# Optimization experiments

Measured on AMD Instinct MI355X. Metric: run time of the kernel, lower is better.

The kernel has to match this reference:

```python
import jax, jax.numpy as jnp
import numpy as np

N, E, D, H = 50000, 800000, 128, 8
DH = D // H  # 16
EPS_LN = 1e-5


def layer_norm(x, gamma, beta):
    mu = jnp.mean(x, axis=-1, keepdims=True)
    var = jnp.var(x, axis=-1, keepdims=True)
    return (x - mu) * jax.lax.rsqrt(var + EPS_LN) * gamma + beta


def setup_inputs() -> dict:
    key = jax.random.key(0)
    ks = jax.random.split(key, 12)
    s = 1.0 / np.sqrt(D)
    x = jax.random.normal(ks[0], (N, D), dtype=jnp.float32)
    src = jax.random.randint(ks[1], (E,), 0, N, dtype=jnp.int32)
    dst = jax.random.randint(ks[2], (E,), 0, N, dtype=jnp.int32)
    Wq = jax.random.normal(ks[3], (D, D), dtype=jnp.float32) * s
    Wk = jax.random.normal(ks[4], (D, D), dtype=jnp.float32) * s
    Wv = jax.random.normal(ks[5], (D, D), dtype=jnp.float32) * s
    Wo = jax.random.normal(ks[6], (D, D), dtype=jnp.float32) * s
    bq = jnp.zeros((D,), jnp.float32)
    bk = jnp.zeros((D,), jnp.float32)
    bv = jnp.zeros((D,), jnp.float32)
    bo = jnp.zeros((D,), jnp.float32)
    gamma1 = jnp.ones((D,), jnp.float32)
    beta1 = jnp.zeros((D,), jnp.float32)
    gamma2 = jnp.ones((D,), jnp.float32)
    beta2 = jnp.zeros((D,), jnp.float32)
    return dict(x=x, src=src, dst=dst, Wq=Wq, bq=bq, Wk=Wk, bk=bk, Wv=Wv, bv=bv,
                Wo=Wo, bo=bo, gamma1=gamma1, beta1=beta1, gamma2=gamma2, beta2=beta2)


def reference(x, src, dst, Wq, bq, Wk, bk, Wv, bv, Wo, bo, gamma1, beta1, gamma2, beta2):
    n = x.shape[0]
    Q = (x @ Wq + bq).reshape(n, H, DH)   # [N,H,Dh]
    K = (x @ Wk + bk).reshape(n, H, DH)
    V = (x @ Wv + bv).reshape(n, H, DH)
    # edge-wise QK dot: score[e,h] = sum_d K[src[e],h,d] * Q[dst[e],h,d]
    score = jnp.sum(K[src] * Q[dst], axis=-1) / np.sqrt(DH)  # [E,H]
    score = jnp.exp(jnp.clip(score, -5.0, 5.0))
    # scatter-sum weighted values and normalizer over destination nodes
    wV = jax.ops.segment_sum(V[src] * score[..., None], dst, num_segments=n)  # [N,H,Dh]
    z = jax.ops.segment_sum(score, dst, num_segments=n)                        # [N,H]
    attn = (wV / (z[..., None] + 1e-3)).reshape(n, D)
    h = layer_norm(x + attn, gamma1, beta1)
    # sublayer: h + relu(O(LN(h)))  (dropout = 0)
    h = h + jax.nn.relu(layer_norm(h, gamma2, beta2) @ Wo + bo)
    return h
```

## Files before the change

kernel.cpp:

```cpp
#include <hip/hip_runtime.h>

typedef unsigned short ushort_t;
typedef __attribute__((ext_vector_type(8))) short short8;
typedef __attribute__((ext_vector_type(4))) float floatx4;
typedef __attribute__((ext_vector_type(2))) _Float16 half2v;
typedef __attribute__((ext_vector_type(8))) _Float16 half8;

#define QSCALE 0.36067376022224085f
#define SCLIP  7.2134752044448170f

__device__ __forceinline__ unsigned h2u(half2v h) {
    union { half2v h; unsigned u; } x; x.h = h; return x.u;
}
__device__ __forceinline__ half2v u2h(unsigned u) {
    union { unsigned u; half2v h; } x; x.u = u; return x.h;
}
__device__ __forceinline__ ushort_t h2us(_Float16 h) {
    union { _Float16 h; ushort_t u; } x; x.h = h; return x.u;
}
__device__ __forceinline__ unsigned pkrtz(float a, float b) {
    auto h = __builtin_amdgcn_cvt_pkrtz(a, b);
    union { decltype(h) h2; unsigned u; } x; x.h2 = h; return x.u;
}
__device__ __forceinline__ float dot2h(half2v a, half2v b, float c) {
#if __has_builtin(__builtin_amdgcn_fdot2)
    return __builtin_amdgcn_fdot2(a, b, c, false);
#else
    return c + (float)a[0] * (float)b[0] + (float)a[1] * (float)b[1];
#endif
}
__device__ __forceinline__ half2v pk_shfl_add(half2v a, int m) {
    unsigned o = (unsigned)__shfl_xor((int)h2u(a), m, 64);
    return a + u2h(o);
}

__global__ __launch_bounds__(256) void transpose_swz(
    const float* __restrict__ Wq, const float* __restrict__ Wk,
    const float* __restrict__ Wv, const float* __restrict__ Wo,
    ushort_t* __restrict__ out, int* __restrict__ deg, int* __restrict__ gcount, int N)
{
    int flat = (blockIdx.y * gridDim.x + blockIdx.x) * 256 + threadIdx.x;
    if (flat == 0) *gcount = 0;
    for (int i = flat; i < N; i += 8192) deg[i] = 0;

    const float* W = (blockIdx.y == 0) ? Wq : (blockIdx.y == 1) ? Wk :
                     (blockIdx.y == 2) ? Wv : Wo;
    ushort_t* T = out + (size_t)blockIdx.y * 128 * 128;
    int t = blockIdx.x * 256 + threadIdx.x;
    int kg = t >> 7;
    int n  = t & 127;
    int k0 = kg * 8;
    float w[8];
    #pragma unroll
    for (int j = 0; j < 8; j++)
        w[j] = W[(size_t)(k0 + j) * 128 + n];
    int4 o;
    o.x = (int)pkrtz(w[0], w[1]);
    o.y = (int)pkrtz(w[2], w[3]);
    o.z = (int)pkrtz(w[4], w[5]);
    o.w = (int)pkrtz(w[6], w[7]);
    int sn = n >> 4, l15 = n & 15, kb = kg >> 2, quad = kg & 3;
    size_t f = ((size_t)((sn * 4 + kb) * 4 + quad)) * 128 + (size_t)l15 * 8;
    *(int4*)(T + f) = o;
}

__global__ __launch_bounds__(512, 8) void gemm_qkv(
    const float* __restrict__ X, const ushort_t* __restrict__ Wsw,
    const float* __restrict__ bq, const float* __restrict__ bk, const float* __restrict__ bv,
    ushort_t* __restrict__ Q, ushort_t* __restrict__ KV, int M,
    const int* __restrict__ dst, int* __restrict__ deg, int* __restrict__ rank, int E)
{
    __shared__ ushort_t Xs[32 * 136];
    __shared__ ushort_t Cs[32 * 392];
    int tid = threadIdx.x;
    int rowBase = blockIdx.x * 32;

    {
        int nblk = gridDim.x;
        int fb = blockIdx.x;
        int per = (E + nblk - 1) / nblk;
        int end = min(per * (fb + 1), E);
        for (int i = per * fb + tid; i < end; i += 512)
            rank[i] = atomicAdd(&deg[dst[i]], 1);
    }

    {
        int r = tid >> 4;
        int c = (tid & 15) * 8;
        int row = rowBase + r;
        int rc = (row < M) ? row : (M - 1);
        const float* p = X + (size_t)rc * 128 + c;
        float4 f0 = *(const float4*)p;
        float4 f1 = *(const float4*)(p + 4);
        int4 pv;
        pv.x = (int)pkrtz(f0.x, f0.y);
        pv.y = (int)pkrtz(f0.z, f0.w);
        pv.z = (int)pkrtz(f1.x, f1.y);
        pv.w = (int)pkrtz(f1.z, f1.w);
        *(int4*)&Xs[r * 136 + c] = pv;
    }
    __syncthreads();

    int lane = tid & 63, wave = tid >> 6;
    int rowT = wave & 1;
    int mg   = wave >> 1;
    int l15 = lane & 15, quad = lane >> 4;
    floatx4 acc[6] = {};
    for (int kb = 0; kb < 4; kb++) {
        half8 a = *(const half8*)&Xs[(rowT * 16 + l15) * 136 + kb * 32 + quad * 8];
        #pragma unroll
        for (int s = 0; s < 6; s++) {
            int ct = mg * 6 + s;
            int mat = ct >> 3;
            int mc  = ct & 7;
            const ushort_t* Wmat = Wsw + (size_t)mat * 128 * 128;
            half8 b = *(const half8*)(Wmat + (size_t)(mc * 4 + kb) * 512 + lane * 8);
            acc[s] = __builtin_amdgcn_mfma_f32_16x16x32_f16(a, b, acc[s], 0, 0, 0);
        }
    }

    #pragma unroll
    for (int s = 0; s < 6; s++) {
        int ct = mg * 6 + s;
        int mat = ct >> 3;
        int col = ct * 16 + l15;
        int matcol = (ct & 7) * 16 + l15;
        const float* bias = (mat == 0) ? bq : (mat == 1) ? bk : bv;
        float bia = bias[matcol];
        float scl = (mat == 0) ? QSCALE : 1.0f;
        for (int rr = 0; rr < 4; rr++) {
            int rl = rowT * 16 + quad * 4 + rr;
            Cs[rl * 392 + col] = h2us((_Float16)((acc[s][rr] + bia) * scl));
        }
    }
    __syncthreads();

    for (int it = 0; it < 3; it++) {
        int idx = it * 512 + tid;
        int rl = idx / 48;
        int sg = idx - rl * 48;
        int row = rowBase + rl;
        if (row < M) {
            short8 v = *(const short8*)&Cs[rl * 392 + sg * 8];
            int gcol = sg * 8;
            int mat = gcol >> 7;
            int mc  = gcol & 127;
            if (mat == 0)
                *(short8*)(Q + (size_t)row * 128 + mc) = v;
            else
                *(short8*)(KV + (size_t)row * 256 + (mc >> 3) * 16 + ((mat == 2) ? 8 : 0)) = v;
        }
    }
}

__global__ __launch_bounds__(256) void k_alloc(const int* __restrict__ deg,
                                               int* __restrict__ offs, int* __restrict__ endp,
                                               int* __restrict__ gcount, int n) {
    __shared__ int s[256];
    __shared__ int base;
    int tid = threadIdx.x;
    int i = blockIdx.x * 256 + tid;
    int v = (i < n) ? deg[i] : 0;
    s[tid] = v;
    __syncthreads();
    for (int d = 1; d < 256; d <<= 1) {
        int t = (tid >= d) ? s[tid - d] : 0;
        __syncthreads();
        s[tid] += t;
        __syncthreads();
    }
    int incl = s[tid];
    if (tid == 255) base = atomicAdd(gcount, incl);
    __syncthreads();
    if (i < n) {
        int o = base + incl - v;
        offs[i] = o;
        endp[i] = o + v;
    }
}

__global__ __launch_bounds__(256) void k_place(const int* __restrict__ src, const int* __restrict__ dst,
                                               const int* __restrict__ rank, const int* __restrict__ offs,
                                               int* __restrict__ eadj, int E) {
    int i = blockIdx.x * 256 + threadIdx.x;
    if (i < E)
        eadj[offs[dst[i]] + rank[i]] = src[i];
}

__global__ __launch_bounds__(256) void edge_attn(
    const ushort_t* __restrict__ Qb, const ushort_t* __restrict__ KV,
    const float* __restrict__ xin,
    const int* __restrict__ offs, const int* __restrict__ endp,
    const int* __restrict__ eadj,
    const float* __restrict__ g1, const float* __restrict__ be1,
    const float* __restrict__ g2, const float* __restrict__ be2,
    ushort_t* __restrict__ h1out, ushort_t* __restrict__ ln2out, int N)
{
    int wave = threadIdx.x >> 6, lane = threadIdx.x & 63;
    int n = blockIdx.x * 4 + wave;
    if (n >= N) return;
    int l15 = lane & 15, grp = lane >> 4;
    int col = l15 * 8 + grp * 2;

    uint4 qp = *(const uint4*)(Qb + (size_t)n * 128 + l15 * 8);
    half2v q0 = u2h(qp.x), q1 = u2h(qp.y), q2 = u2h(qp.z), q3 = u2h(qp.w);

    int s0 = offs[n], s1 = endp[n];

    float2 xv  = *(const float2*)(xin + (size_t)n * 128 + col);
    float2 gv  = *(const float2*)(g1 + col);
    float2 bvv = *(const float2*)(be1 + col);
    float2 g2v = *(const float2*)(g2 + col);
    float2 b2v = *(const float2*)(be2 + col);

    half2v a01 = u2h(0u), a23 = u2h(0u), a45 = u2h(0u), a67 = u2h(0u);
    float z = 0.f;
    for (int base = s0; base < s1; base += 64) {
        int cnt = min(s1 - base, 64);
        int ee = (base + lane < s1) ? eadj[base + lane] : 0;

        auto comp = [&](uint4 kk, uint4 vv, int jj) {
            float d = dot2h(u2h(kk.x), q0,
                      dot2h(u2h(kk.y), q1,
                      dot2h(u2h(kk.z), q2,
                      dot2h(u2h(kk.w), q3, 0.f))));
            d += __shfl_xor(d, 1, 64);
            float sc = fminf(SCLIP, fmaxf(-SCLIP, d));
            float e = (jj < cnt) ? exp2f(sc) : 0.f;
            _Float16 eh = (_Float16)e;
            half2v ep; ep[0] = eh; ep[1] = eh;
            a01 += u2h(vv.x) * ep;
            a23 += u2h(vv.y) * ep;
            a45 += u2h(vv.z) * ep;
            a67 += u2h(vv.w) * ep;
            z += e;
        };

        for (int j0 = 0; j0 < cnt; j0 += 16) {
            int t0 = j0 + grp;
            int sn0 = __shfl(ee, t0, 64);
            int sn1 = __shfl(ee, t0 + 4, 64);
            int sn2 = __shfl(ee, t0 + 8, 64);
            int sn3 = __shfl(ee, t0 + 12, 64);
            const ushort_t* p0 = KV + (size_t)sn0 * 256 + l15 * 16;
            const ushort_t* p1 = KV + (size_t)sn1 * 256 + l15 * 16;
            const ushort_t* p2 = KV + (size_t)sn2 * 256 + l15 * 16;
            const ushort_t* p3 = KV + (size_t)sn3 * 256 + l15 * 16;
            uint4 kk0 = *(const uint4*)p0, vv0 = *(const uint4*)(p0 + 8);
            uint4 kk1 = *(const uint4*)p1, vv1 = *(const uint4*)(p1 + 8);
            uint4 kk2 = *(const uint4*)p2, vv2 = *(const uint4*)(p2 + 8);
            uint4 kk3 = *(const uint4*)p3, vv3 = *(const uint4*)(p3 + 8);
            comp(kk0, vv0, t0);
            comp(kk1, vv1, t0 + 4);
            comp(kk2, vv2, t0 + 8);
            comp(kk3, vv3, t0 + 12);
        }
    }
    a01 = pk_shfl_add(a01, 16); a01 = pk_shfl_add(a01, 32);
    a23 = pk_shfl_add(a23, 16); a23 = pk_shfl_add(a23, 32);
    a45 = pk_shfl_add(a45, 16); a45 = pk_shfl_add(a45, 32);
    a67 = pk_shfl_add(a67, 16); a67 = pk_shfl_add(a67, 32);
    z += __shfl_xor(z, 16, 64); z += __shfl_xor(z, 32, 64);
    float inv = 1.f / (z + 1e-3f);

    half2v ap = (grp == 0) ? a01 : (grp == 1) ? a23 : (grp == 2) ? a45 : a67;
    float a0 = (float)ap[0], a1 = (float)ap[1];

    float t0 = fmaf(a0, inv, xv.x);
    float t1 = fmaf(a1, inv, xv.y);

    float s = t0 + t1, s2 = t0 * t0 + t1 * t1;
    #pragma unroll
    for (int m = 1; m < 64; m <<= 1) { s += __shfl_xor(s, m, 64); s2 += __shfl_xor(s2, m, 64); }
    float mu = s * (1.f / 128.f);
    float var = s2 * (1.f / 128.f) - mu * mu;
    float rstd = rsqrtf(var + 1e-5f);

    float h0 = (t0 - mu) * rstd * gv.x + bvv.x;
    float h1 = (t1 - mu) * rstd * gv.y + bvv.y;
    *(unsigned*)(h1out + (size_t)n * 128 + col) = pkrtz(h0, h1);

    s = h0 + h1; s2 = h0 * h0 + h1 * h1;
    #pragma unroll
    for (int m = 1; m < 64; m <<= 1) { s += __shfl_xor(s, m, 64); s2 += __shfl_xor(s2, m, 64); }
    float mu2 = s * (1.f / 128.f);
    float var2 = s2 * (1.f / 128.f) - mu2 * mu2;
    float rstd2 = rsqrtf(var2 + 1e-5f);

    float l0 = (h0 - mu2) * rstd2 * g2v.x + b2v.x;
    float l1 = (h1 - mu2) * rstd2 * g2v.y + b2v.y;
    *(unsigned*)(ln2out + (size_t)n * 128 + col) = pkrtz(l0, l1);
}

__global__ __launch_bounds__(256) void gemm_o(
    const ushort_t* __restrict__ X, const ushort_t* __restrict__ Wsw,
    const float* __restrict__ bo, const ushort_t* __restrict__ h1in,
    float* __restrict__ Out, int M)
{
    __shared__ ushort_t As[64 * 136];
    int tid = threadIdx.x;
    int rowBase = blockIdx.x * 64;
    int snBase = blockIdx.y * 4;
    int colBase = snBase * 16;

    int r = tid >> 4;
    int c = (tid & 15) * 8;
    for (int rr = 0; rr < 64; rr += 16) {
        int row = rowBase + rr + r;
        int rc = (row < M) ? row : (M - 1);
        short8 v = *(const short8*)(X + (size_t)rc * 128 + c);
        *(short8*)&As[(rr + r) * 136 + c] = v;
    }
    __syncthreads();

    int lane = tid & 63, wave = tid >> 6;
    int wm = wave * 16;
    int l15 = lane & 15, quad = lane >> 4;
    floatx4 acc[4] = {};
    for (int kb = 0; kb < 4; kb++) {
        half8 a = *(const half8*)&As[(wm + l15) * 136 + kb * 32 + quad * 8];
        for (int s = 0; s < 4; s++) {
            half8 b = *(const half8*)(Wsw + (size_t)((snBase + s) * 4 + kb) * 512 + lane * 8);
            acc[s] = __builtin_amdgcn_mfma_f32_16x16x32_f16(a, b, acc[s], 0, 0, 0);
        }
    }

    float* Cs = (float*)As;
    for (int s = 0; s < 4; s++) {
        int cl = s * 16 + l15;
        float bia = bo[colBase + cl];
        for (int rr2 = 0; rr2 < 4; rr2++) {
            int rl = wm + quad * 4 + rr2;
            Cs[rl * 68 + cl] = fmaxf(acc[s][rr2] + bia, 0.f);
        }
    }
    for (int it = 0; it < 4; it++) {
        int idx = it * 64 + lane;
        int rl = idx >> 4;
        int c4 = (idx & 15) * 4;
        int row = rowBase + wm + rl;
        if (row < M) {
            float4 v = *(const float4*)&Cs[(wm + rl) * 68 + c4];
            uint2 hp = *(const uint2*)(h1in + (size_t)row * 128 + colBase + c4);
            half2v ha = u2h(hp.x), hb = u2h(hp.y);
            v.x += (float)ha[0];
            v.y += (float)ha[1];
            v.z += (float)hb[0];
            v.w += (float)hb[1];
            *(float4*)(Out + (size_t)row * 128 + colBase + c4) = v;
        }
    }
}

extern "C" void kernel_launch(void* const* d_in, const int* in_sizes, int n_in,
                              void* d_out, int out_size, void* d_ws, size_t ws_size,
                              hipStream_t stream) {
    const int D = 128;
    const int N = in_sizes[0] / D;
    const int E = in_sizes[1];

    const float* x   = (const float*)d_in[0];
    const int*   src = (const int*)d_in[1];
    const int*   dst = (const int*)d_in[2];
    const float* Wq  = (const float*)d_in[3];
    const float* bq  = (const float*)d_in[4];
    const float* Wk  = (const float*)d_in[5];
    const float* bk  = (const float*)d_in[6];
    const float* Wv  = (const float*)d_in[7];
    const float* bv  = (const float*)d_in[8];
    const float* Wo  = (const float*)d_in[9];
    const float* bo  = (const float*)d_in[10];
    const float* g1  = (const float*)d_in[11];
    const float* be1 = (const float*)d_in[12];
    const float* g2  = (const float*)d_in[13];
    const float* be2 = (const float*)d_in[14];

    char* ws = (char*)d_ws;
    size_t o = 0;
    auto alloc = [&](size_t b) { o = (o + 255) & ~(size_t)255; size_t r = o; o += b; return r; };
    ushort_t* Qb   = (ushort_t*)(ws + alloc((size_t)N * D * 2));
    ushort_t* KVb  = (ushort_t*)(ws + alloc((size_t)N * D * 4));
    ushort_t* ln2  = (ushort_t*)(ws + alloc((size_t)N * D * 2));
    ushort_t* h1   = (ushort_t*)(ws + alloc((size_t)N * D * 2));
    ushort_t* Wt   = (ushort_t*)(ws + alloc((size_t)4 * 128 * 128 * 2));
    int*      deg  = (int*)(ws + alloc((size_t)N * 4));
    int*      offs = (int*)(ws + alloc((size_t)(N + 1) * 4));
    int*      endp = (int*)(ws + alloc((size_t)N * 4));
    int*      gcnt = (int*)(ws + alloc((size_t)256 * 4));
    int*      eadj = (int*)(ws + alloc((size_t)E * 4));
    int*      rank = (int*)(ws + alloc((size_t)E * 4));

    int nScanBlocks = (N + 255) / 256;
    int nEdgeBlocks = (E + 255) / 256;
    int nRowTiles32 = (N + 31) / 32;
    int nRowTiles = (N + 63) / 64;

    transpose_swz<<<dim3(8, 4), 256, 0, stream>>>(Wq, Wk, Wv, Wo, Wt, deg, gcnt, N);
    gemm_qkv<<<nRowTiles32, 512, 0, stream>>>(x, Wt, bq, bk, bv, Qb, KVb, N, dst, deg, rank, E);
    k_alloc<<<nScanBlocks, 256, 0, stream>>>(deg, offs, endp, gcnt, N);
    k_place<<<nEdgeBlocks, 256, 0, stream>>>(src, dst, rank, offs, eadj, E);
    edge_attn<<<(N + 3) / 4, 256, 0, stream>>>(Qb, KVb, x, offs, endp, eadj, g1, be1, g2, be2, h1, ln2, N);
    gemm_o<<<dim3(nRowTiles, 2), 256, 0, stream>>>(ln2, Wt + 3 * 128 * 128, bo, h1, (float*)d_out, N);
}
```

Measured before the change: 238.0 us.

## Split KV rows into K and V halves and retile output GEMM

The KV buffer layout changes from interleaved per-head K/V 16-element chunks to a contiguous K half followed by a V half. Each lane in the edge attention loop now reads 16 bytes from each half, so neighbouring lanes touch contiguous K (and contiguous V) memory. The output GEMM is reorganised into 32-row tiles with 512 threads, each block covering all 128 columns. This removes the second grid dimension and the duplicated X tile loads. The aim is better coalescing of the gathered KV rows and less redundant traffic in the final GEMM, at the cost of two separate 256-byte segments per gathered row.

```diff
diff --git a/kernel.cpp b/kernel.cpp
--- a/kernel.cpp
+++ b/kernel.cpp
@@ -148,7 +148,7 @@
             if (mat == 0)
                 *(short8*)(Q + (size_t)row * 128 + mc) = v;
             else
-                *(short8*)(KV + (size_t)row * 256 + (mc >> 3) * 16 + ((mat == 2) ? 8 : 0)) = v;
+                *(short8*)(KV + (size_t)row * 256 + ((mat == 2) ? 128 : 0) + mc) = v;
         }
     }
 }
@@ -242,14 +242,14 @@
             int sn1 = __shfl(ee, t0 + 4, 64);
             int sn2 = __shfl(ee, t0 + 8, 64);
             int sn3 = __shfl(ee, t0 + 12, 64);
-            const ushort_t* p0 = KV + (size_t)sn0 * 256 + l15 * 16;
-            const ushort_t* p1 = KV + (size_t)sn1 * 256 + l15 * 16;
-            const ushort_t* p2 = KV + (size_t)sn2 * 256 + l15 * 16;
-            const ushort_t* p3 = KV + (size_t)sn3 * 256 + l15 * 16;
-            uint4 kk0 = *(const uint4*)p0, vv0 = *(const uint4*)(p0 + 8);
-            uint4 kk1 = *(const uint4*)p1, vv1 = *(const uint4*)(p1 + 8);
-            uint4 kk2 = *(const uint4*)p2, vv2 = *(const uint4*)(p2 + 8);
-            uint4 kk3 = *(const uint4*)p3, vv3 = *(const uint4*)(p3 + 8);
+            const ushort_t* p0 = KV + (size_t)sn0 * 256 + l15 * 8;
+            const ushort_t* p1 = KV + (size_t)sn1 * 256 + l15 * 8;
+            const ushort_t* p2 = KV + (size_t)sn2 * 256 + l15 * 8;
+            const ushort_t* p3 = KV + (size_t)sn3 * 256 + l15 * 8;
+            uint4 kk0 = *(const uint4*)p0, vv0 = *(const uint4*)(p0 + 128);
+            uint4 kk1 = *(const uint4*)p1, vv1 = *(const uint4*)(p1 + 128);
+            uint4 kk2 = *(const uint4*)p2, vv2 = *(const uint4*)(p2 + 128);
+            uint4 kk3 = *(const uint4*)p3, vv3 = *(const uint4*)(p3 + 128);
             comp(kk0, vv0, t0);
             comp(kk1, vv1, t0 + 4);
             comp(kk2, vv2, t0 + 8);
@@ -292,62 +292,65 @@
     *(unsigned*)(ln2out + (size_t)n * 128 + col) = pkrtz(l0, l1);
 }
 
-__global__ __launch_bounds__(256) void gemm_o(
+__global__ __launch_bounds__(512, 8) void gemm_o(
     const ushort_t* __restrict__ X, const ushort_t* __restrict__ Wsw,
     const float* __restrict__ bo, const ushort_t* __restrict__ h1in,
     float* __restrict__ Out, int M)
 {
-    __shared__ ushort_t As[64 * 136];
+    __shared__ ushort_t Xs[32 * 136];
+    __shared__ float Cs[32 * 132];
     int tid = threadIdx.x;
-    int rowBase = blockIdx.x * 64;
-    int snBase = blockIdx.y * 4;
-    int colBase = snBase * 16;
-
-    int r = tid >> 4;
-    int c = (tid & 15) * 8;
-    for (int rr = 0; rr < 64; rr += 16) {
-        int row = rowBase + rr + r;
+    int rowBase = blockIdx.x * 32;
+
+    {
+        int r = tid >> 4;
+        int c = (tid & 15) * 8;
+        int row = rowBase + r;
         int rc = (row < M) ? row : (M - 1);
-        short8 v = *(const short8*)(X + (size_t)rc * 128 + c);
-        *(short8*)&As[(rr + r) * 136 + c] = v;
+        *(short8*)&Xs[r * 136 + c] = *(const short8*)(X + (size_t)rc * 128 + c);
     }
     __syncthreads();
 
     int lane = tid & 63, wave = tid >> 6;
-    int wm = wave * 16;
+    int rowT = wave & 1;
+    int cg   = wave >> 1;
     int l15 = lane & 15, quad = lane >> 4;
-    floatx4 acc[4] = {};
+    floatx4 acc[2] = {};
     for (int kb = 0; kb < 4; kb++) {
-        half8 a = *(const half8*)&As[(wm + l15) * 136 + kb * 32 + quad * 8];
-        for (int s = 0; s < 4; s++) {
-            half8 b = *(const half8*)(Wsw + (size_t)((snBase + s) * 4 + kb) * 512 + lane * 8);
+        half8 a = *(const half8*)&Xs[(rowT * 16 + l15) * 136 + kb * 32 + quad * 8];
+        #pragma unroll
+        for (int s = 0; s < 2; s++) {
+            int sn = cg * 2 + s;
+            half8 b = *(const half8*)(Wsw + (size_t)(sn * 4 + kb) * 512 + lane * 8);
             acc[s] = __builtin_amdgcn_mfma_f32_16x16x32_f16(a, b, acc[s], 0, 0, 0);
         }
     }
 
-    float* Cs = (float*)As;
-    for (int s = 0; s < 4; s++) {
-        int cl = s * 16 + l15;
-        float bia = bo[colBase + cl];
-        for (int rr2 = 0; rr2 < 4; rr2++) {
-            int rl = wm + quad * 4 + rr2;
-            Cs[rl * 68 + cl] = fmaxf(acc[s][rr2] + bia, 0.f);
-        }
-    }
-    for (int it = 0; it < 4; it++) {
-        int idx = it * 64 + lane;
-        int rl = idx >> 4;
-        int c4 = (idx & 15) * 4;
-        int row = rowBase + wm + rl;
+    #pragma unroll
+    for (int s = 0; s < 2; s++) {
+        int cl = (cg * 2 + s) * 16 + l15;
+        float bia = bo[cl];
+        for (int rr = 0; rr < 4; rr++) {
+            int rl = rowT * 16 + quad * 4 + rr;
+            Cs[rl * 132 + cl] = fmaxf(acc[s][rr] + bia, 0.f);
+        }
+    }
+    __syncthreads();
+
+    for (int it = 0; it < 2; it++) {
+        int idx = it * 512 + tid;
+        int rl = idx >> 5;
+        int c4 = (idx & 31) * 4;
+        int row = rowBase + rl;
         if (row < M) {
-            float4 v = *(const float4*)&Cs[(wm + rl) * 68 + c4];
-            uint2 hp = *(const uint2*)(h1in + (size_t)row * 128 + colBase + c4);
+            float4 v = *(const float4*)&Cs[rl * 132 + c4];
+            uint2 hp = *(const uint2*)(h1in + (size_t)row * 128 + c4);
             half2v ha = u2h(hp.x), hb = u2h(hp.y);
             v.x += (float)ha[0];
             v.y += (float)ha[1];
             v.z += (float)hb[0];
             v.w += (float)hb[1];
-            *(float4*)(Out + (size_t)row * 128 + colBase + c4) = v;
+            *(float4*)(Out + (size_t)row * 128 + c4) = v;
         }
     }
 }
@@ -393,12 +396,11 @@
     int nScanBlocks = (N + 255) / 256;
     int nEdgeBlocks = (E + 255) / 256;
     int nRowTiles32 = (N + 31) / 32;
-    int nRowTiles = (N + 63) / 64;
 
     transpose_swz<<<dim3(8, 4), 256, 0, stream>>>(Wq, Wk, Wv, Wo, Wt, deg, gcnt, N);
     gemm_qkv<<<nRowTiles32, 512, 0, stream>>>(x, Wt, bq, bk, bv, Qb, KVb, N, dst, deg, rank, E);
     k_alloc<<<nScanBlocks, 256, 0, stream>>>(deg, offs, endp, gcnt, N);
     k_place<<<nEdgeBlocks, 256, 0, stream>>>(src, dst, rank, offs, eadj, E);
     edge_attn<<<(N + 3) / 4, 256, 0, stream>>>(Qb, KVb, x, offs, endp, eadj, g1, be1, g2, be2, h1, ln2, N);
-    gemm_o<<<dim3(nRowTiles, 2), 256, 0, stream>>>(ln2, Wt + 3 * 128 * 128, bo, h1, (float*)d_out, N);
-}
+    gemm_o<<<nRowTiles32, 512, 0, stream>>>(ln2, Wt + 3 * 128 * 128, bo, h1, (float*)d_out, N);
+}
```

After: 233.7 us. About the same (-1.8%).
